# Kernel optimization log

Hardware: AMD Instinct MI355X
Metric: run time of the kernel (lower is better)

## Reference

```python
import jax, jax.numpy as jnp
import numpy as np

N = 131072      # 8192 sudoku puzzles x 16 cells
E = 1048576     # random constraint edges (avg degree 8)
HID = 64
NEG_SLOPE = 0.2


def setup_inputs() -> dict:
    key = jax.random.key(0)
    ks = jax.random.split(key, 18)
    p = lambda k, shape: jax.random.normal(k, shape, dtype=jnp.float32) * 0.05
    return {
        "x": jax.random.randint(ks[0], (N,), 0, 5),
        "edge_index": jax.random.randint(ks[1], (2, E), 0, N),
        "emb": p(ks[2], (5, HID)),
        # conv1: in 64 -> heads=4, C=64, concat
        "W1": p(ks[3], (HID, 4 * HID)),
        "a1_src": p(ks[4], (4, HID)),
        "a1_dst": p(ks[5], (4, HID)),
        "b1": p(ks[6], (4 * HID,)),
        # conv2: in 256 -> heads=4, C=64, concat
        "W2": p(ks[7], (4 * HID, 4 * HID)),
        "a2_src": p(ks[8], (4, HID)),
        "a2_dst": p(ks[9], (4, HID)),
        "b2": p(ks[10], (4 * HID,)),
        # conv3: in 256 -> heads=1, C=64, no concat
        "W3": p(ks[11], (4 * HID, HID)),
        "a3_src": p(ks[12], (1, HID)),
        "a3_dst": p(ks[13], (1, HID)),
        "b3": p(ks[14], (HID,)),
        "fc_w": p(ks[15], (HID, 5)),
        "fc_b": p(ks[16], (5,)),
    }


def gat_conv(x, src, dst, W, a_src, a_dst, b, concat):
    """PyG-style GATConv (self-loops already appended to src/dst)."""
    n = x.shape[0]
    H, C = a_src.shape
    h = (x @ W).reshape(n, H, C)                       # [N,H,C]
    alpha_s = jnp.einsum('nhc,hc->nh', h, a_src)       # [N,H]
    alpha_d = jnp.einsum('nhc,hc->nh', h, a_dst)
    e = jax.nn.leaky_relu(alpha_s[src] + alpha_d[dst], NEG_SLOPE)  # [E,H]
    # scatter-softmax over incoming edges per destination node
    e_max = jax.ops.segment_max(e, dst, num_segments=n)
    e_exp = jnp.exp(e - e_max[dst])
    denom = jax.ops.segment_sum(e_exp, dst, num_segments=n)
    alpha = e_exp / (denom[dst] + 1e-16)               # [E,H]
    msg = h[src] * alpha[:, :, None]                   # [E,H,C]
    out = jax.ops.segment_sum(msg, dst, num_segments=n)  # [N,H,C]
    out = out.reshape(n, H * C) if concat else out.mean(axis=1)
    return out + b


def reference(x, edge_index, emb, W1, a1_src, a1_dst, b1,
              W2, a2_src, a2_dst, b2, W3, a3_src, a3_dst, b3, fc_w, fc_b):
    n = x.shape[0]
    loops = jnp.arange(n)
    src = jnp.concatenate([edge_index[0], loops])  # add self-loops (PyG default)
    dst = jnp.concatenate([edge_index[1], loops])
    h = emb[x]                                                    # [N,64]
    h = jax.nn.elu(gat_conv(h, src, dst, W1, a1_src, a1_dst, b1, True))
    h = jax.nn.elu(gat_conv(h, src, dst, W2, a2_src, a2_dst, b2, True))
    h = jax.nn.elu(gat_conv(h, src, dst, W3, a3_src, a3_dst, b3, False))
    return h @ fc_w + fc_b                                        # [N,5]
```

## Files before the change

### kernel.cpp

```cpp
#include <hip/hip_runtime.h>
#include <hip/hip_bf16.h>
#include <hip/hip_fp8.h>

typedef __attribute__((ext_vector_type(8))) short short8;
typedef __attribute__((ext_vector_type(4))) short short4_t;
typedef __attribute__((ext_vector_type(4))) float floatx4;
typedef __attribute__((ext_vector_type(2))) float floatx2;

constexpr int NB  = 256;
constexpr int CAP = 6144;

__device__ __forceinline__ unsigned short f2bf(float f){
  unsigned int u = __float_as_uint(f);
  u += 0x7FFF + ((u >> 16) & 1);
  return (unsigned short)(u >> 16);
}
__device__ __forceinline__ float bf2f(unsigned short h){
  return __uint_as_float(((unsigned int)h) << 16);
}
__device__ __forceinline__ float lrelu(float x){ return x > 0.f ? x : 0.2f * x; }
__device__ __forceinline__ float eluf(float x){ return x > 0.f ? x : (__expf(x) - 1.f); }

__device__ __forceinline__ unsigned char f2fp8(float f){
  __hip_fp8_e4m3 t(f);
  return (unsigned char)t.__x;
}
__device__ __forceinline__ float fp82f(unsigned char b){
  __hip_fp8_e4m3 t;
  t.__x = (__hip_fp8_storage_t)b;
  return (float)t;
}

template<bool HI>
__device__ __forceinline__ floatx2 fp8pk2(unsigned int v){
#if defined(__has_builtin) && __has_builtin(__builtin_amdgcn_cvt_pk_f32_fp8)
  return __builtin_amdgcn_cvt_pk_f32_fp8((int)v, HI);
#else
  floatx2 r;
  constexpr int sh = HI ? 16 : 0;
  r.x = fp82f((unsigned char)((v >> sh) & 0xFF));
  r.y = fp82f((unsigned char)((v >> (sh + 8)) & 0xFF));
  return r;
#endif
}

__device__ __forceinline__ unsigned int f32x4_to_fp8(float a0, float a1, float a2, float a3){
#if defined(__has_builtin) && __has_builtin(__builtin_amdgcn_cvt_pk_fp8_f32)
  int w = 0;
  w = __builtin_amdgcn_cvt_pk_fp8_f32(a0, a1, w, false);
  w = __builtin_amdgcn_cvt_pk_fp8_f32(a2, a3, w, true);
  return (unsigned int)w;
#else
  return (unsigned int)f2fp8(a0) | ((unsigned int)f2fp8(a1) << 8) |
         ((unsigned int)f2fp8(a2) << 16) | ((unsigned int)f2fp8(a3) << 24);
#endif
}

__device__ __forceinline__ int scr512(int p){
  int q = p >> 2, s = p & 3;
  int qq = ((q & 31) << 2) | (q >> 5);
  return (qq << 2) | s;
}

__device__ __forceinline__ void gload16(const unsigned short* g, unsigned short* l){
  __builtin_amdgcn_global_load_lds(
      (const __attribute__((address_space(1))) unsigned int*)(const void*)g,
      (__attribute__((address_space(3))) unsigned int*)(void*)l,
      16, 0, 0);
}

__global__ __launch_bounds__(256) void part_prep_k(const int* __restrict__ ei, int E, int shift,
                                                   int* __restrict__ gcnt,
                                                   uint2* __restrict__ bbuf, int PB,
                                                   const float* __restrict__ W2,
                                                   unsigned short* __restrict__ Wp2,
                                                   const float* __restrict__ W3,
                                                   unsigned short* __restrict__ Wp3,
                                                   const float* __restrict__ emb,
                                                   const float* __restrict__ W1,
                                                   const float* __restrict__ a1s,
                                                   const float* __restrict__ a1d,
                                                   float* __restrict__ T1,
                                                   float* __restrict__ wt_tab){
  int blk = blockIdx.x;
  int tid = threadIdx.x;
  if (blk < PB){
    __shared__ int hist[NB];
    __shared__ int base[NB];
    hist[tid] = 0;
    __syncthreads();
    int blk_start = blk * 4096;
    int src[16], bkt[16], lp[16];
    #pragma unroll
    for (int k = 0; k < 16; k++){
      int i = blk_start + k * 256 + tid;
      if (i < E){
        int dst = ei[E + i];
        src[k] = ei[i];
        bkt[k] = dst >> shift;
        lp[k] = atomicAdd(&hist[bkt[k]], 1);
      } else {
        bkt[k] = -1;
      }
    }
    __syncthreads();
    base[tid] = atomicAdd(&gcnt[tid], hist[tid]);
    __syncthreads();
    #pragma unroll
    for (int k = 0; k < 16; k++){
      int i = blk_start + k * 256 + tid;
      if (i < E){
        int b = bkt[k];
        int dst = ei[E + i];
        bbuf[(size_t)b * CAP + base[b] + lp[k]] = make_uint2((unsigned)src[k], (unsigned)dst);
      }
    }
    return;
  }
  int b = blk - PB;
  if (b < 256){
    int idx = b * 256 + tid;
    int k = idx >> 8, nn = idx & 255;
    Wp2[nn * 256 + k] = f2bf(W2[idx]);
  } else if (b < 320){
    int idx = (b - 256) * 256 + tid;
    int k = idx >> 6, nn = idx & 63;
    Wp3[nn * 256 + k] = f2bf(W3[idx]);
  } else {
    __shared__ float t_lds[1280];
    __shared__ float as_l[20], ad_l[20];
    for (int i = tid; i < 1280; i += 256){
      int r = i >> 8, c = i & 255;
      float s = 0.f;
      for (int k = 0; k < 64; k++) s += emb[r * 64 + k] * W1[k * 256 + c];
      t_lds[i] = s;
      T1[i] = s;
    }
    __syncthreads();
    if (tid < 20){
      int r = tid >> 2, hh = tid & 3;
      float ss = 0.f, sd = 0.f;
      for (int c = 0; c < 64; c++){
        float f = t_lds[r * 256 + hh * 64 + c];
        ss += f * a1s[hh * 64 + c];
        sd += f * a1d[hh * 64 + c];
      }
      as_l[tid] = ss;
      ad_l[tid] = sd;
    }
    __syncthreads();
    if (tid < 100){
      int xd = tid / 20, rest = tid % 20;
      int h = rest & 3;
      wt_tab[tid] = __expf(lrelu(as_l[rest] + ad_l[xd * 4 + h]));
    }
  }
}

__global__ __launch_bounds__(256) void bscan_k(const int* __restrict__ gcnt,
                                               int* __restrict__ gbase,
                                               int* __restrict__ row_ptr, int N, int dpb){
  __shared__ int s[NB];
  int t = threadIdx.x;
  int v = gcnt[t] + dpb;
  s[t] = v;
  __syncthreads();
  #pragma unroll
  for (int off = 1; off < NB; off <<= 1){
    int u = (t >= off) ? s[t - off] : 0;
    __syncthreads();
    s[t] += u;
    __syncthreads();
  }
  gbase[t] = s[t] - v;
  if (t == NB - 1){ gbase[NB] = s[t]; row_ptr[N] = s[t]; }
}

__global__ __launch_bounds__(256) void sort_k(const uint2* __restrict__ bbuf,
                                              const int* __restrict__ gcnt,
                                              const int* __restrict__ gbase,
                                              int* __restrict__ row_ptr,
                                              int* __restrict__ sorted_src,
                                              int* __restrict__ perm, int dpb){
  __shared__ int counts[512];
  __shared__ int curs[512];
  __shared__ int wsum[256];
  __shared__ int sortedL[CAP + 512];
  __shared__ int dh[64];
  int b = blockIdx.x, tid = threadIdx.x;
  int cnt = gcnt[b];
  int dstBase = b * dpb;
  int gb = gbase[b];
  counts[tid] = 0;
  counts[tid + 256] = 0;
  __syncthreads();
  for (int i = tid; i < cnt; i += 256){
    uint2 p = bbuf[(size_t)b * CAP + i];
    atomicAdd(&counts[(int)p.y - dstBase], 1);
  }
  __syncthreads();
  int c0 = counts[2 * tid] + 1;
  int c1 = counts[2 * tid + 1] + 1;
  int sum = c0 + c1;
  wsum[tid] = sum;
  __syncthreads();
  #pragma unroll
  for (int off = 1; off < 256; off <<= 1){
    int u = (tid >= off) ? wsum[tid - off] : 0;
    __syncthreads();
    wsum[tid] += u;
    __syncthreads();
  }
  int ex = wsum[tid] - sum;
  int ro0 = ex, ro1 = ex + c0;
  curs[2 * tid] = ro0 + 1;
  curs[2 * tid + 1] = ro1 + 1;
  sortedL[ro0] = dstBase + 2 * tid;
  sortedL[ro1] = dstBase + 2 * tid + 1;
  row_ptr[dstBase + 2 * tid] = gb + ro0;
  row_ptr[dstBase + 2 * tid + 1] = gb + ro1;
  __syncthreads();
  for (int i = tid; i < cnt; i += 256){
    uint2 p = bbuf[(size_t)b * CAP + i];
    int pos = atomicAdd(&curs[(int)p.y - dstBase], 1);
    sortedL[pos] = (int)p.x;
  }
  __syncthreads();
  int tot = cnt + dpb;
  for (int i = tid; i < tot; i += 256) sorted_src[gb + i] = sortedL[i];

  __syncthreads();
  if (tid < 64) dh[tid] = 0;
  __syncthreads();
  int dg0 = c0 < 63 ? c0 : 63;
  int dg1 = c1 < 63 ? c1 : 63;
  int r0 = atomicAdd(&dh[dg0], 1);
  int r1 = atomicAdd(&dh[dg1], 1);
  __syncthreads();
  if (tid == 0){
    int run = 0;
    for (int i = 0; i < 64; i++){ int c = dh[i]; dh[i] = run; run += c; }
  }
  __syncthreads();
  perm[dstBase + scr512(dh[dg0] + r0)] = dstBase + 2 * tid;
  perm[dstBase + scr512(dh[dg1] + r1)] = dstBase + 2 * tid + 1;
}

template<int BN, int MODE, bool F8OUT>
__global__ __launch_bounds__(256) void gemm_lds_k(const unsigned short* __restrict__ A,
                                                  const unsigned short* __restrict__ Wp,
                                                  void* __restrict__ Cout, int Nc,
                                                  const float* __restrict__ a_src,
                                                  const float* __restrict__ a_dst,
                                                  float* __restrict__ as_arr,
                                                  float* __restrict__ ad_arr){
  constexpr int K = 256;
  constexpr int NT = BN / 32;
  __shared__ unsigned short Alds[128 * 32];
  __shared__ unsigned short Blds[BN * 32];
  __shared__ float asl[128], adl[128];
  __shared__ float pas[128][2], pad[128][2];
  int tid = threadIdx.x;
  int w = tid >> 6, l = tid & 63;
  int r16 = l & 15, quad = l >> 4;
  int wr = w >> 1, wc = w & 1;
  int mBase = blockIdx.x * 128;
  int nBase = blockIdx.y * BN;

  if constexpr (MODE == 1){
    if (tid < 128){ asl[tid] = a_src[nBase + tid]; adl[tid] = a_dst[nBase + tid]; }
  }
  if constexpr (MODE == 2){
    if (tid < 64){ asl[tid] = a_src[tid]; adl[tid] = a_dst[tid]; }
  }

  int arow = l >> 2;
  int kcol = (l & 3) * 8;
  const unsigned short* gA0 = A + (size_t)(mBase + w * 32 + arow) * K + kcol;
  const unsigned short* gA1 = gA0 + (size_t)16 * K;
  unsigned short* lA0 = &Alds[(w * 32) * 32];
  unsigned short* lA1 = &Alds[(w * 32 + 16) * 32];
  const unsigned short* gB0;
// ... 73 lines not shown
          float v = acc[mt][nt][r];
          int ci = wc * 64 + nt * 16 + r16;
          ps += v * asl[ci];
          pd += v * adl[ci];
        }
        ps += __shfl_xor(ps, 1, 64); ps += __shfl_xor(ps, 2, 64);
        ps += __shfl_xor(ps, 4, 64); ps += __shfl_xor(ps, 8, 64);
        pd += __shfl_xor(pd, 1, 64); pd += __shfl_xor(pd, 2, 64);
        pd += __shfl_xor(pd, 4, 64); pd += __shfl_xor(pd, 8, 64);
        if (r16 == 0){
          int row = mBase + wr * 64 + mt * 16 + quad * 4 + r;
          as_arr[row * 4 + head] = ps;
          ad_arr[row * 4 + head] = pd;
        }
      }
    }
  }
  if constexpr (MODE == 2){
    #pragma unroll
    for (int mt = 0; mt < 4; mt++){
      #pragma unroll
      for (int r = 0; r < 4; r++){
        float ps = 0.f, pd = 0.f;
        #pragma unroll
        for (int nt = 0; nt < NT; nt++){
          float v = acc[mt][nt][r];
          int ci = wc * 32 + nt * 16 + r16;
          ps += v * asl[ci];
          pd += v * adl[ci];
        }
        ps += __shfl_xor(ps, 1, 64); ps += __shfl_xor(ps, 2, 64);
        ps += __shfl_xor(ps, 4, 64); ps += __shfl_xor(ps, 8, 64);
        pd += __shfl_xor(pd, 1, 64); pd += __shfl_xor(pd, 2, 64);
        pd += __shfl_xor(pd, 4, 64); pd += __shfl_xor(pd, 8, 64);
        if (r16 == 0){
          int lr = wr * 64 + mt * 16 + quad * 4 + r;
          pas[lr][wc] = ps;
          pad[lr][wc] = pd;
        }
      }
    }
    __syncthreads();
    if (tid < 128){
      as_arr[mBase + tid] = pas[tid][0] + pas[tid][1];
      ad_arr[mBase + tid] = pad[tid][0] + pad[tid][1];
    }
  }
}


__global__ __launch_bounds__(256) void agg1_k(const int* __restrict__ x,
                                              const float* __restrict__ T1,
                                              const float* __restrict__ wt_tab,
                                              const int* __restrict__ row_ptr,
                                              const int* __restrict__ sorted_src,
                                              const int* __restrict__ perm,
                                              const float* __restrict__ bias,
                                              unsigned short* __restrict__ outb){
  __shared__ float t_lds[1280];
  __shared__ float wt_l[100], b_lds[256];
  __shared__ float cnt_lds[256][5];
  __shared__ int xd_lds[256];
  __shared__ int dd_lds[256];
  int tid = threadIdx.x;
  for (int i = tid; i < 1280; i += 256) t_lds[i] = T1[i];
  if (tid < 100) wt_l[tid] = wt_tab[tid];
  b_lds[tid] = bias[tid];
  int gi = blockIdx.x * 256 + tid;
  int d = perm[(gi & ~511) + scr512(gi & 511)];
  int start = row_ptr[d], end = row_ptr[d + 1];
  xd_lds[tid] = x[d];
  dd_lds[tid] = d;
  float c0 = 0.f, c1 = 0.f, c2 = 0.f, c3 = 0.f, c4 = 0.f;
  for (int e = start; e < end; e++){
    int xs = x[sorted_src[e]];
    c0 += (xs == 0) ? 1.f : 0.f;
    c1 += (xs == 1) ? 1.f : 0.f;
    c2 += (xs == 2) ? 1.f : 0.f;
    c3 += (xs == 3) ? 1.f : 0.f;
    c4 += (xs == 4) ? 1.f : 0.f;
  }
  cnt_lds[tid][0] = c0; cnt_lds[tid][1] = c1; cnt_lds[tid][2] = c2;
  cnt_lds[tid][3] = c3; cnt_lds[tid][4] = c4;
  __syncthreads();
  int w = tid >> 6, l = tid & 63;
  int head = l >> 4;
  int c0i = l * 4;
  for (int dl = w; dl < 256; dl += 4){
    int dd = dd_lds[dl];
    int xd20 = xd_lds[dl] * 20;
    float ws[5];
    float den = 0.f;
    #pragma unroll
    for (int v2 = 0; v2 < 5; v2++){
      float wv = wt_l[xd20 + v2 * 4 + head] * cnt_lds[dl][v2];
      ws[v2] = wv;
      den += wv;
    }
    float inv = 1.f / (den + 1e-16f);
    float num[4] = {0.f, 0.f, 0.f, 0.f};
    #pragma unroll
    for (int v2 = 0; v2 < 5; v2++){
      const float4 row = *(const float4*)&t_lds[v2 * 256 + c0i];
      num[0] += ws[v2] * row.x;
      num[1] += ws[v2] * row.y;
      num[2] += ws[v2] * row.z;
      num[3] += ws[v2] * row.w;
    }
    short4_t ov;
    #pragma unroll
    for (int j = 0; j < 4; j++)
      ov[j] = (short)f2bf(eluf(num[j] * inv + b_lds[c0i + j]));
    *(short4_t*)(outb + (size_t)dd * 256 + c0i) = ov;
  }
}


__global__ __launch_bounds__(256) void agg4_k(const unsigned char* __restrict__ h8,
                                              const float* __restrict__ as_arr,
                                              const float* __restrict__ ad_arr,
                                              const int* __restrict__ row_ptr,
                                              const int* __restrict__ sorted_src,
                                              const int* __restrict__ perm,
                                              const float* __restrict__ bias,
                                              unsigned short* __restrict__ outb){
  int tid = threadIdx.x;
  int w = tid >> 6, l = tid & 63;
  int g = l >> 4, q = l & 15;
  int d = perm[blockIdx.x * 16 + w * 4 + g];
  unsigned coff = (unsigned)(q * 16);
  int head = q >> 2;
  int start = row_ptr[d], end = row_ptr[d + 1];
  float a_d = ad_arr[d * 4 + head];
  floatx2 ac[8];
  #pragma unroll
  for (int j = 0; j < 8; j++){ floatx2 z = {0.f, 0.f}; ac[j] = z; }
  float den = 0.f;
  int e = start;
  for (; e + 3 < end; e += 4){
    unsigned s0 = (unsigned)sorted_src[e];
    unsigned s1 = (unsigned)sorted_src[e + 1];
    unsigned s2 = (unsigned)sorted_src[e + 2];
    unsigned s3 = (unsigned)sorted_src[e + 3];
    uint4 v0 = *(const uint4*)(h8 + (((size_t)s0 << 8) | coff));
    uint4 v1 = *(const uint4*)(h8 + (((size_t)s1 << 8) | coff));
    uint4 v2 = *(const uint4*)(h8 + (((size_t)s2 << 8) | coff));
    uint4 v3 = *(const uint4*)(h8 + (((size_t)s3 << 8) | coff));
    float w0 = __expf(lrelu(as_arr[(s0 << 2) + head] + a_d));
    float w1 = __expf(lrelu(as_arr[(s1 << 2) + head] + a_d));
    float w2 = __expf(lrelu(as_arr[(s2 << 2) + head] + a_d));
    float w3 = __expf(lrelu(as_arr[(s3 << 2) + head] + a_d));
    den += (w0 + w1) + (w2 + w3);
    floatx2 W0 = {w0, w0}, W1 = {w1, w1}, W2 = {w2, w2}, W3 = {w3, w3};
    ac[0] += W0 * fp8pk2<false>(v0.x) + W1 * fp8pk2<false>(v1.x)
           + W2 * fp8pk2<false>(v2.x) + W3 * fp8pk2<false>(v3.x);
    ac[1] += W0 * fp8pk2<true>(v0.x)  + W1 * fp8pk2<true>(v1.x)
           + W2 * fp8pk2<true>(v2.x)  + W3 * fp8pk2<true>(v3.x);
    ac[2] += W0 * fp8pk2<false>(v0.y) + W1 * fp8pk2<false>(v1.y)
           + W2 * fp8pk2<false>(v2.y) + W3 * fp8pk2<false>(v3.y);
    ac[3] += W0 * fp8pk2<true>(v0.y)  + W1 * fp8pk2<true>(v1.y)
           + W2 * fp8pk2<true>(v2.y)  + W3 * fp8pk2<true>(v3.y);
    ac[4] += W0 * fp8pk2<false>(v0.z) + W1 * fp8pk2<false>(v1.z)
           + W2 * fp8pk2<false>(v2.z) + W3 * fp8pk2<false>(v3.z);
    ac[5] += W0 * fp8pk2<true>(v0.z)  + W1 * fp8pk2<true>(v1.z)
           + W2 * fp8pk2<true>(v2.z)  + W3 * fp8pk2<true>(v3.z);
    ac[6] += W0 * fp8pk2<false>(v0.w) + W1 * fp8pk2<false>(v1.w)
           + W2 * fp8pk2<false>(v2.w) + W3 * fp8pk2<false>(v3.w);
    ac[7] += W0 * fp8pk2<true>(v0.w)  + W1 * fp8pk2<true>(v1.w)
           + W2 * fp8pk2<true>(v2.w)  + W3 * fp8pk2<true>(v3.w);
  }
  for (; e < end; e++){
    unsigned s = (unsigned)sorted_src[e];
    uint4 v = *(const uint4*)(h8 + (((size_t)s << 8) | coff));
    float wg = __expf(lrelu(as_arr[(s << 2) + head] + a_d));
    den += wg;
    floatx2 wv = {wg, wg};
    ac[0] += wv * fp8pk2<false>(v.x);
    ac[1] += wv * fp8pk2<true>(v.x);
    ac[2] += wv * fp8pk2<false>(v.y);
    ac[3] += wv * fp8pk2<true>(v.y);
    ac[4] += wv * fp8pk2<false>(v.z);
    ac[5] += wv * fp8pk2<true>(v.z);
    ac[6] += wv * fp8pk2<false>(v.w);
    ac[7] += wv * fp8pk2<true>(v.w);
  }
  float inv = 0.015625f / (den + 1e-16f);
  int cb = q * 16;
  float4 b0 = *(const float4*)&bias[cb];
  float4 b1v = *(const float4*)&bias[cb + 4];
  float4 b2v = *(const float4*)&bias[cb + 8];
  float4 b3v = *(const float4*)&bias[cb + 12];
  float bb[16] = {b0.x, b0.y, b0.z, b0.w, b1v.x, b1v.y, b1v.z, b1v.w,
                  b2v.x, b2v.y, b2v.z, b2v.w, b3v.x, b3v.y, b3v.z, b3v.w};
  short8 o0, o1;
  #pragma unroll
  for (int j = 0; j < 8; j++){
    float v = ((j & 1) ? ac[j >> 1].y : ac[j >> 1].x);
    o0[j] = (short)f2bf(eluf(v * inv + bb[j]));
  }
  #pragma unroll
  for (int j = 0; j < 8; j++){
    float v = ((j & 1) ? ac[4 + (j >> 1)].y : ac[4 + (j >> 1)].x);
    o1[j] = (short)f2bf(eluf(v * inv + bb[8 + j]));
  }
  *(short8*)(outb + (size_t)d * 256 + cb) = o0;
  *(short8*)(outb + (size_t)d * 256 + cb + 8) = o1;
}


__global__ __launch_bounds__(256) void agg3_k(const unsigned char* __restrict__ h8,
                                              const float* __restrict__ as_arr,
                                              const float* __restrict__ ad_arr,
                                              const int* __restrict__ row_ptr,
                                              const int* __restrict__ sorted_src,
                                              const int* __restrict__ perm,
                                              const float* __restrict__ bias,
                                              unsigned short* __restrict__ outb){
  int tid = threadIdx.x;
  int w = tid >> 6, l = tid & 63;
  int g = l >> 3, q = l & 7;
  int d = perm[blockIdx.x * 32 + w * 8 + g];
  unsigned coff = (unsigned)(q * 8);
  int start = row_ptr[d], end = row_ptr[d + 1];
  float a_d = ad_arr[d];
  floatx2 ac[4];
  #pragma unroll
  for (int j = 0; j < 4; j++){ floatx2 z = {0.f, 0.f}; ac[j] = z; }
  float den = 0.f;
  int e = start;
  for (; e + 3 < end; e += 4){
    unsigned s0 = (unsigned)sorted_src[e];
    unsigned s1 = (unsigned)sorted_src[e + 1];
    unsigned s2 = (unsigned)sorted_src[e + 2];
    unsigned s3 = (unsigned)sorted_src[e + 3];
    uint2 v0 = *(const uint2*)(h8 + (((size_t)s0 << 6) | coff));
    uint2 v1 = *(const uint2*)(h8 + (((size_t)s1 << 6) | coff));
    uint2 v2 = *(const uint2*)(h8 + (((size_t)s2 << 6) | coff));
    uint2 v3 = *(const uint2*)(h8 + (((size_t)s3 << 6) | coff));
    float w0 = __expf(lrelu(as_arr[s0] + a_d));
    float w1 = __expf(lrelu(as_arr[s1] + a_d));
    float w2 = __expf(lrelu(as_arr[s2] + a_d));
    float w3 = __expf(lrelu(as_arr[s3] + a_d));
    den += (w0 + w1) + (w2 + w3);
    floatx2 W0 = {w0, w0}, W1 = {w1, w1}, W2 = {w2, w2}, W3 = {w3, w3};
    ac[0] += W0 * fp8pk2<false>(v0.x) + W1 * fp8pk2<false>(v1.x)
           + W2 * fp8pk2<false>(v2.x) + W3 * fp8pk2<false>(v3.x);
    ac[1] += W0 * fp8pk2<true>(v0.x)  + W1 * fp8pk2<true>(v1.x)
           + W2 * fp8pk2<true>(v2.x)  + W3 * fp8pk2<true>(v3.x);
    ac[2] += W0 * fp8pk2<false>(v0.y) + W1 * fp8pk2<false>(v1.y)
           + W2 * fp8pk2<false>(v2.y) + W3 * fp8pk2<false>(v3.y);
    ac[3] += W0 * fp8pk2<true>(v0.y)  + W1 * fp8pk2<true>(v1.y)
           + W2 * fp8pk2<true>(v2.y)  + W3 * fp8pk2<true>(v3.y);
  }
  for (; e < end; e++){
    unsigned s = (unsigned)sorted_src[e];
    float wg = __expf(lrelu(as_arr[s] + a_d));
    den += wg;
    uint2 v = *(const uint2*)(h8 + (((size_t)s << 6) | coff));
    floatx2 wv = {wg, wg};
    ac[0] += wv * fp8pk2<false>(v.x);
    ac[1] += wv * fp8pk2<true>(v.x);
    ac[2] += wv * fp8pk2<false>(v.y);
    ac[3] += wv * fp8pk2<true>(v.y);
  }
  float inv = 0.015625f / (den + 1e-16f);
  int cb = q * 8;
  float4 bA = *(const float4*)&bias[cb];
  float4 bB = *(const float4*)&bias[cb + 4];
  float bb[8] = {bA.x, bA.y, bA.z, bA.w, bB.x, bB.y, bB.z, bB.w};
  short8 ov;
  #pragma unroll
  for (int j = 0; j < 8; j++){
    float v = ((j & 1) ? ac[j >> 1].y : ac[j >> 1].x);
    ov[j] = (short)f2bf(eluf(v * inv + bb[j]));
  }
  *(short8*)(outb + (size_t)d * 64 + cb) = ov;
}


__global__ __launch_bounds__(256) void fc_k(const unsigned short* __restrict__ hb,
                                            const float* __restrict__ fcw,
                                            const float* __restrict__ fcb,
                                            float* __restrict__ out){
  __shared__ float w_lds[320];
  __shared__ float b_lds[5];
  int tid = threadIdx.x;
  for (int i = tid; i < 320; i += 256) w_lds[i] = fcw[i];
  if (tid < 5) b_lds[tid] = fcb[tid];
  __syncthreads();
  int n = blockIdx.x * 256 + tid;
  const short8* p = (const short8*)(hb + (size_t)n * 64);
  float acc[5];
  #pragma unroll
  for (int j = 0; j < 5; j++) acc[j] = b_lds[j];
  #pragma unroll
  for (int b = 0; b < 8; b++){
    short8 v = p[b];
    #pragma unroll
    for (int j8 = 0; j8 < 8; j8++){
      float f = bf2f((unsigned short)v[j8]);
      int k = b * 8 + j8;
      #pragma unroll
      for (int j = 0; j < 5; j++) acc[j] += f * w_lds[k * 5 + j];
    }
  }
  #pragma unroll
  for (int j = 0; j < 5; j++) out[(size_t)n * 5 + j] = acc[j];
}


extern "C" void kernel_launch(void* const* d_in, const int* in_sizes, int n_in,
                              void* d_out, int out_size, void* d_ws, size_t ws_size,
                              hipStream_t stream){
  const int*   x    = (const int*)d_in[0];
  const int*   ei   = (const int*)d_in[1];
  const float* emb  = (const float*)d_in[2];
  const float* W1   = (const float*)d_in[3];
  const float* a1s  = (const float*)d_in[4];
  const float* a1d  = (const float*)d_in[5];
  const float* b1   = (const float*)d_in[6];
  const float* W2   = (const float*)d_in[7];
  const float* a2s  = (const float*)d_in[8];
  const float* a2d  = (const float*)d_in[9];
  const float* b2   = (const float*)d_in[10];
  const float* W3   = (const float*)d_in[11];
  const float* a3s  = (const float*)d_in[12];
  const float* a3d  = (const float*)d_in[13];
  const float* b3   = (const float*)d_in[14];
  const float* fcw  = (const float*)d_in[15];
  const float* fcb  = (const float*)d_in[16];
  float* out = (float*)d_out;

  const int N = in_sizes[0];
  const int E = in_sizes[1] / 2;
  const int dpb = N / NB;
  int shift = 0;
  while ((1 << shift) < dpb) shift++;
  const int PB = (E + 4095) / 4096;

  char* base = (char*)d_ws;
  size_t off = 0;
  auto alloc = [&](size_t bytes) -> void* {
    void* p = base + off;
    off += (bytes + 255) & ~(size_t)255;
    return p;
  };
  unsigned short* bufB    = (unsigned short*)alloc((size_t)N * 256 * 2);
  unsigned char*  buf8    = (unsigned char*)alloc((size_t)N * 256);
  float* alpha_s          = (float*)alloc((size_t)N * 4 * 4);
  float* alpha_d          = (float*)alloc((size_t)N * 4 * 4);
  int* row_ptr            = (int*)alloc((size_t)(N + 1) * 4);
  int* sorted_src         = (int*)alloc((size_t)(E + N) * 4);
  int* perm               = (int*)alloc((size_t)N * 4);
  uint2* bbuf             = (uint2*)alloc((size_t)NB * CAP * 8);
  int* gcnt               = (int*)alloc((size_t)NB * 4);
  int* gbase              = (int*)alloc((size_t)(NB + 1) * 4);
  float* T1               = (float*)alloc(5 * 256 * 4);
  float* wt_tab           = (float*)alloc(100 * 4);
  unsigned short* Wp2     = (unsigned short*)alloc(256 * 256 * 2);
  unsigned short* Wp3     = (unsigned short*)alloc(64 * 256 * 2);

  (void)hipMemsetAsync(gcnt, 0, (size_t)NB * 4, stream);
  part_prep_k<<<PB + 321, 256, 0, stream>>>(ei, E, shift, gcnt, bbuf, PB,
                                            W2, Wp2, W3, Wp3, emb, W1, a1s, a1d, T1, wt_tab);
  bscan_k<<<1, 256, 0, stream>>>(gcnt, gbase, row_ptr, N, dpb);
  sort_k<<<NB, 256, 0, stream>>>(bbuf, gcnt, gbase, row_ptr, sorted_src, perm, dpb);

  agg1_k<<<N / 256, 256, 0, stream>>>(x, T1, wt_tab, row_ptr, sorted_src, perm, b1, bufB);

  gemm_lds_k<128, 1, true><<<dim3(N / 128, 2), 256, 0, stream>>>(bufB, Wp2, buf8, 256,
                                                                 a2s, a2d, alpha_s, alpha_d);
  agg4_k<<<N / 16, 256, 0, stream>>>(buf8, alpha_s, alpha_d, row_ptr, sorted_src, perm, b2, bufB);

  gemm_lds_k<64, 2, true><<<dim3(N / 128, 1), 256, 0, stream>>>(bufB, Wp3, buf8, 64,
                                                                a3s, a3d, alpha_s, alpha_d);
  agg3_k<<<N / 32, 256, 0, stream>>>(buf8, alpha_s, alpha_d, row_ptr, sorted_src, perm, b3, bufB);

  fc_k<<<N / 256, 256, 0, stream>>>(bufB, fcw, fcb, out);
}
```

Measured before the change: 333.6 us.

## Cooperative shuffle-broadcast edge index loads and persistent grids in aggregation kernels

Result: slower. 360.2 us (+8.0%).

```diff
diff --git a/kernel.cpp b/kernel.cpp
--- a/kernel.cpp
+++ b/kernel.cpp
@@ -427,7 +427,18 @@
   xd_lds[tid] = x[d];
   dd_lds[tid] = d;
   float c0 = 0.f, c1 = 0.f, c2 = 0.f, c3 = 0.f, c4 = 0.f;
-  for (int e = start; e < end; e++){
+  int e = start;
+  for (; e + 3 < end; e += 4){
+    int s0 = sorted_src[e], s1 = sorted_src[e + 1];
+    int s2 = sorted_src[e + 2], s3 = sorted_src[e + 3];
+    int x0 = x[s0], x1 = x[s1], x2 = x[s2], x3 = x[s3];
+    c0 += (float)((x0 == 0) + (x1 == 0) + (x2 == 0) + (x3 == 0));
+    c1 += (float)((x0 == 1) + (x1 == 1) + (x2 == 1) + (x3 == 1));
+    c2 += (float)((x0 == 2) + (x1 == 2) + (x2 == 2) + (x3 == 2));
+    c3 += (float)((x0 == 3) + (x1 == 3) + (x2 == 3) + (x3 == 3));
+    c4 += (float)((x0 == 4) + (x1 == 4) + (x2 == 4) + (x3 == 4));
+  }
+  for (; e < end; e++){
     int xs = x[sorted_src[e]];
     c0 += (xs == 0) ? 1.f : 0.f;
     c1 += (xs == 1) ? 1.f : 0.f;
@@ -478,88 +489,87 @@
                                               const int* __restrict__ sorted_src,
                                               const int* __restrict__ perm,
                                               const float* __restrict__ bias,
-                                              unsigned short* __restrict__ outb){
+                                              unsigned short* __restrict__ outb,
+                                              int nBlk){
   int tid = threadIdx.x;
   int w = tid >> 6, l = tid & 63;
   int g = l >> 4, q = l & 15;
-  int d = perm[blockIdx.x * 16 + w * 4 + g];
+  int sl0 = l & 48;
   unsigned coff = (unsigned)(q * 16);
   int head = q >> 2;
-  int start = row_ptr[d], end = row_ptr[d + 1];
-  float a_d = ad_arr[d * 4 + head];
-  floatx2 ac[8];
-  #pragma unroll
-  for (int j = 0; j < 8; j++){ floatx2 z = {0.f, 0.f}; ac[j] = z; }
-  float den = 0.f;
-  int e = start;
-  for (; e + 3 < end; e += 4){
-    unsigned s0 = (unsigned)sorted_src[e];
-    unsigned s1 = (unsigned)sorted_src[e + 1];
-    unsigned s2 = (unsigned)sorted_src[e + 2];
-    unsigned s3 = (unsigned)sorted_src[e + 3];
-    uint4 v0 = *(const uint4*)(h8 + (((size_t)s0 << 8) | coff));
-    uint4 v1 = *(const uint4*)(h8 + (((size_t)s1 << 8) | coff));
-    uint4 v2 = *(const uint4*)(h8 + (((size_t)s2 << 8) | coff));
-    uint4 v3 = *(const uint4*)(h8 + (((size_t)s3 << 8) | coff));
-    float w0 = __expf(lrelu(as_arr[(s0 << 2) + head] + a_d));
-    float w1 = __expf(lrelu(as_arr[(s1 << 2) + head] + a_d));
-    float w2 = __expf(lrelu(as_arr[(s2 << 2) + head] + a_d));
-    float w3 = __expf(lrelu(as_arr[(s3 << 2) + head] + a_d));
-    den += (w0 + w1) + (w2 + w3);
-    floatx2 W0 = {w0, w0}, W1 = {w1, w1}, W2 = {w2, w2}, W3 = {w3, w3};
-    ac[0] += W0 * fp8pk2<false>(v0.x) + W1 * fp8pk2<false>(v1.x)
-           + W2 * fp8pk2<false>(v2.x) + W3 * fp8pk2<false>(v3.x);
-    ac[1] += W0 * fp8pk2<true>(v0.x)  + W1 * fp8pk2<true>(v1.x)
-           + W2 * fp8pk2<true>(v2.x)  + W3 * fp8pk2<true>(v3.x);
-    ac[2] += W0 * fp8pk2<false>(v0.y) + W1 * fp8pk2<false>(v1.y)
-           + W2 * fp8pk2<false>(v2.y) + W3 * fp8pk2<false>(v3.y);
-    ac[3] += W0 * fp8pk2<true>(v0.y)  + W1 * fp8pk2<true>(v1.y)
-           + W2 * fp8pk2<true>(v2.y)  + W3 * fp8pk2<true>(v3.y);
-    ac[4] += W0 * fp8pk2<false>(v0.z) + W1 * fp8pk2<false>(v1.z)
-           + W2 * fp8pk2<false>(v2.z) + W3 * fp8pk2<false>(v3.z);
-    ac[5] += W0 * fp8pk2<true>(v0.z)  + W1 * fp8pk2<true>(v1.z)
-           + W2 * fp8pk2<true>(v2.z)  + W3 * fp8pk2<true>(v3.z);
-    ac[6] += W0 * fp8pk2<false>(v0.w) + W1 * fp8pk2<false>(v1.w)
-           + W2 * fp8pk2<false>(v2.w) + W3 * fp8pk2<false>(v3.w);
-    ac[7] += W0 * fp8pk2<true>(v0.w)  + W1 * fp8pk2<true>(v1.w)
-           + W2 * fp8pk2<true>(v2.w)  + W3 * fp8pk2<true>(v3.w);
-  }
-  for (; e < end; e++){
-    unsigned s = (unsigned)sorted_src[e];
-    uint4 v = *(const uint4*)(h8 + (((size_t)s << 8) | coff));
-    float wg = __expf(lrelu(as_arr[(s << 2) + head] + a_d));
-    den += wg;
-    floatx2 wv = {wg, wg};
-    ac[0] += wv * fp8pk2<false>(v.x);
-    ac[1] += wv * fp8pk2<true>(v.x);
-    ac[2] += wv * fp8pk2<false>(v.y);
-    ac[3] += wv * fp8pk2<true>(v.y);
-    ac[4] += wv * fp8pk2<false>(v.z);
-    ac[5] += wv * fp8pk2<true>(v.z);
-    ac[6] += wv * fp8pk2<false>(v.w);
-    ac[7] += wv * fp8pk2<true>(v.w);
-  }
-  float inv = 0.015625f / (den + 1e-16f);
   int cb = q * 16;
-  float4 b0 = *(const float4*)&bias[cb];
-  float4 b1v = *(const float4*)&bias[cb + 4];
-  float4 b2v = *(const float4*)&bias[cb + 8];
-  float4 b3v = *(const float4*)&bias[cb + 12];
-  float bb[16] = {b0.x, b0.y, b0.z, b0.w, b1v.x, b1v.y, b1v.z, b1v.w,
-                  b2v.x, b2v.y, b2v.z, b2v.w, b3v.x, b3v.y, b3v.z, b3v.w};
-  short8 o0, o1;
-  #pragma unroll
-  for (int j = 0; j < 8; j++){
-    float v = ((j & 1) ? ac[j >> 1].y : ac[j >> 1].x);
-    o0[j] = (short)f2bf(eluf(v * inv + bb[j]));
-  }
-  #pragma unroll
-  for (int j = 0; j < 8; j++){
-    float v = ((j & 1) ? ac[4 + (j >> 1)].y : ac[4 + (j >> 1)].x);
-    o1[j] = (short)f2bf(eluf(v * inv + bb[8 + j]));
-  }
-  *(short8*)(outb + (size_t)d * 256 + cb) = o0;
-  *(short8*)(outb + (size_t)d * 256 + cb + 8) = o1;
+  float4 bv0 = *(const float4*)&bias[cb];
+  float4 bv1 = *(const float4*)&bias[cb + 4];
+  float4 bv2 = *(const float4*)&bias[cb + 8];
+  float4 bv3 = *(const float4*)&bias[cb + 12];
+  float bb[16] = {bv0.x, bv0.y, bv0.z, bv0.w, bv1.x, bv1.y, bv1.z, bv1.w,
+                  bv2.x, bv2.y, bv2.z, bv2.w, bv3.x, bv3.y, bv3.z, bv3.w};
+
+  for (int blk = blockIdx.x; blk < nBlk; blk += gridDim.x){
+    int d = perm[blk * 16 + w * 4 + g];
+    int start = row_ptr[d], end = row_ptr[d + 1];
+    float a_d = ad_arr[d * 4 + head];
+    floatx2 ac[8];
+    #pragma unroll
+    for (int j = 0; j < 8; j++){ floatx2 z = {0.f, 0.f}; ac[j] = z; }
+    float den = 0.f;
+
+    for (int base = start; base < end; base += 16){
+      int myE = base + q;
+      int idxl = (myE < end) ? sorted_src[myE] : 0;
+      #pragma unroll
+      for (int sb = 0; sb < 4; sb++){
+        int eb = base + sb * 4;
+        if (eb < end){
+          unsigned s0 = (unsigned)__shfl(idxl, sl0 + sb * 4 + 0, 64);
+          unsigned s1 = (unsigned)__shfl(idxl, sl0 + sb * 4 + 1, 64);
+          unsigned s2 = (unsigned)__shfl(idxl, sl0 + sb * 4 + 2, 64);
+          unsigned s3 = (unsigned)__shfl(idxl, sl0 + sb * 4 + 3, 64);
+          uint4 v0 = *(const uint4*)(h8 + (((size_t)s0 << 8) | coff));
+          uint4 v1 = *(const uint4*)(h8 + (((size_t)s1 << 8) | coff));
+          uint4 v2 = *(const uint4*)(h8 + (((size_t)s2 << 8) | coff));
+          uint4 v3 = *(const uint4*)(h8 + (((size_t)s3 << 8) | coff));
+          float w0 = (eb + 0 < end) ? __expf(lrelu(as_arr[(s0 << 2) + head] + a_d)) : 0.f;
+          float w1 = (eb + 1 < end) ? __expf(lrelu(as_arr[(s1 << 2) + head] + a_d)) : 0.f;
+          float w2 = (eb + 2 < end) ? __expf(lrelu(as_arr[(s2 << 2) + head] + a_d)) : 0.f;
+          float w3 = (eb + 3 < end) ? __expf(lrelu(as_arr[(s3 << 2) + head] + a_d)) : 0.f;
+          den += (w0 + w1) + (w2 + w3);
+          floatx2 W0 = {w0, w0}, W1 = {w1, w1}, W2 = {w2, w2}, W3 = {w3, w3};
+          ac[0] += W0 * fp8pk2<false>(v0.x) + W1 * fp8pk2<false>(v1.x)
+                 + W2 * fp8pk2<false>(v2.x) + W3 * fp8pk2<false>(v3.x);
+          ac[1] += W0 * fp8pk2<true>(v0.x)  + W1 * fp8pk2<true>(v1.x)
+                 + W2 * fp8pk2<true>(v2.x)  + W3 * fp8pk2<true>(v3.x);
+          ac[2] += W0 * fp8pk2<false>(v0.y) + W1 * fp8pk2<false>(v1.y)
+                 + W2 * fp8pk2<false>(v2.y) + W3 * fp8pk2<false>(v3.y);
+          ac[3] += W0 * fp8pk2<true>(v0.y)  + W1 * fp8pk2<true>(v1.y)
+                 + W2 * fp8pk2<true>(v2.y)  + W3 * fp8pk2<true>(v3.y);
+          ac[4] += W0 * fp8pk2<false>(v0.z) + W1 * fp8pk2<false>(v1.z)
+                 + W2 * fp8pk2<false>(v2.z) + W3 * fp8pk2<false>(v3.z);
+          ac[5] += W0 * fp8pk2<true>(v0.z)  + W1 * fp8pk2<true>(v1.z)
+                 + W2 * fp8pk2<true>(v2.z)  + W3 * fp8pk2<true>(v3.z);
+          ac[6] += W0 * fp8pk2<false>(v0.w) + W1 * fp8pk2<false>(v1.w)
+                 + W2 * fp8pk2<false>(v2.w) + W3 * fp8pk2<false>(v3.w);
+          ac[7] += W0 * fp8pk2<true>(v0.w)  + W1 * fp8pk2<true>(v1.w)
+                 + W2 * fp8pk2<true>(v2.w)  + W3 * fp8pk2<true>(v3.w);
+        }
+      }
+    }
+
+    float inv = 0.015625f / (den + 1e-16f);
+    short8 o0, o1;
+    #pragma unroll
+    for (int j = 0; j < 8; j++){
+      float v = ((j & 1) ? ac[j >> 1].y : ac[j >> 1].x);
+      o0[j] = (short)f2bf(eluf(v * inv + bb[j]));
+    }
+    #pragma unroll
+    for (int j = 0; j < 8; j++){
+      float v = ((j & 1) ? ac[4 + (j >> 1)].y : ac[4 + (j >> 1)].x);
+      o1[j] = (short)f2bf(eluf(v * inv + bb[8 + j]));
+    }
+    *(short8*)(outb + (size_t)d * 256 + cb) = o0;
+    *(short8*)(outb + (size_t)d * 256 + cb + 8) = o1;
+  }
 }
 
 
@@ -570,66 +580,69 @@
                                               const int* __restrict__ sorted_src,
                                               const int* __restrict__ perm,
                                               const float* __restrict__ bias,
-                                              unsigned short* __restrict__ outb){
+                                              unsigned short* __restrict__ outb,
+                                              int nBlk){
   int tid = threadIdx.x;
   int w = tid >> 6, l = tid & 63;
   int g = l >> 3, q = l & 7;
-  int d = perm[blockIdx.x * 32 + w * 8 + g];
+  int sl0 = l & 56;
   unsigned coff = (unsigned)(q * 8);
-  int start = row_ptr[d], end = row_ptr[d + 1];
-  float a_d = ad_arr[d];
-  floatx2 ac[4];
-  #pragma unroll
-  for (int j = 0; j < 4; j++){ floatx2 z = {0.f, 0.f}; ac[j] = z; }
-  float den = 0.f;
-  int e = start;
-  for (; e + 3 < end; e += 4){
-    unsigned s0 = (unsigned)sorted_src[e];
-    unsigned s1 = (unsigned)sorted_src[e + 1];
-    unsigned s2 = (unsigned)sorted_src[e + 2];
-    unsigned s3 = (unsigned)sorted_src[e + 3];
-    uint2 v0 = *(const uint2*)(h8 + (((size_t)s0 << 6) | coff));
-    uint2 v1 = *(const uint2*)(h8 + (((size_t)s1 << 6) | coff));
-    uint2 v2 = *(const uint2*)(h8 + (((size_t)s2 << 6) | coff));
-    uint2 v3 = *(const uint2*)(h8 + (((size_t)s3 << 6) | coff));
-    float w0 = __expf(lrelu(as_arr[s0] + a_d));
-    float w1 = __expf(lrelu(as_arr[s1] + a_d));
-    float w2 = __expf(lrelu(as_arr[s2] + a_d));
-    float w3 = __expf(lrelu(as_arr[s3] + a_d));
-    den += (w0 + w1) + (w2 + w3);
-    floatx2 W0 = {w0, w0}, W1 = {w1, w1}, W2 = {w2, w2}, W3 = {w3, w3};
-    ac[0] += W0 * fp8pk2<false>(v0.x) + W1 * fp8pk2<false>(v1.x)
-           + W2 * fp8pk2<false>(v2.x) + W3 * fp8pk2<false>(v3.x);
-    ac[1] += W0 * fp8pk2<true>(v0.x)  + W1 * fp8pk2<true>(v1.x)
-           + W2 * fp8pk2<true>(v2.x)  + W3 * fp8pk2<true>(v3.x);
-    ac[2] += W0 * fp8pk2<false>(v0.y) + W1 * fp8pk2<false>(v1.y)
-           + W2 * fp8pk2<false>(v2.y) + W3 * fp8pk2<false>(v3.y);
-    ac[3] += W0 * fp8pk2<true>(v0.y)  + W1 * fp8pk2<true>(v1.y)
-           + W2 * fp8pk2<true>(v2.y)  + W3 * fp8pk2<true>(v3.y);
-  }
-  for (; e < end; e++){
-    unsigned s = (unsigned)sorted_src[e];
-    float wg = __expf(lrelu(as_arr[s] + a_d));
-    den += wg;
-    uint2 v = *(const uint2*)(h8 + (((size_t)s << 6) | coff));
-    floatx2 wv = {wg, wg};
-    ac[0] += wv * fp8pk2<false>(v.x);
-    ac[1] += wv * fp8pk2<true>(v.x);
-    ac[2] += wv * fp8pk2<false>(v.y);
-    ac[3] += wv * fp8pk2<true>(v.y);
-  }
-  float inv = 0.015625f / (den + 1e-16f);
   int cb = q * 8;
   float4 bA = *(const float4*)&bias[cb];
   float4 bB = *(const float4*)&bias[cb + 4];
   float bb[8] = {bA.x, bA.y, bA.z, bA.w, bB.x, bB.y, bB.z, bB.w};
-  short8 ov;
-  #pragma unroll
-  for (int j = 0; j < 8; j++){
-    float v = ((j & 1) ? ac[j >> 1].y : ac[j >> 1].x);
-    ov[j] = (short)f2bf(eluf(v * inv + bb[j]));
-  }
-  *(short8*)(outb + (size_t)d * 64 + cb) = ov;
+
+  for (int blk = blockIdx.x; blk < nBlk; blk += gridDim.x){
+    int d = perm[blk * 32 + w * 8 + g];
+    int start = row_ptr[d], end = row_ptr[d + 1];
+    float a_d = ad_arr[d];
+    floatx2 ac[4];
+    #pragma unroll
+    for (int j = 0; j < 4; j++){ floatx2 z = {0.f, 0.f}; ac[j] = z; }
+    float den = 0.f;
+
+    for (int base = start; base < end; base += 8){
+      int myE = base + q;
+      int idxl = (myE < end) ? sorted_src[myE] : 0;
+      #pragma unroll
+      for (int sb = 0; sb < 2; sb++){
+        int eb = base + sb * 4;
+        if (eb < end){
+          unsigned s0 = (unsigned)__shfl(idxl, sl0 + sb * 4 + 0, 64);
+          unsigned s1 = (unsigned)__shfl(idxl, sl0 + sb * 4 + 1, 64);
+          unsigned s2 = (unsigned)__shfl(idxl, sl0 + sb * 4 + 2, 64);
+          unsigned s3 = (unsigned)__shfl(idxl, sl0 + sb * 4 + 3, 64);
+          uint2 v0 = *(const uint2*)(h8 + (((size_t)s0 << 6) | coff));
+          uint2 v1 = *(const uint2*)(h8 + (((size_t)s1 << 6) | coff));
+          uint2 v2 = *(const uint2*)(h8 + (((size_t)s2 << 6) | coff));
+          uint2 v3 = *(const uint2*)(h8 + (((size_t)s3 << 6) | coff));
+          float w0 = (eb + 0 < end) ? __expf(lrelu(as_arr[s0] + a_d)) : 0.f;
+          float w1 = (eb + 1 < end) ? __expf(lrelu(as_arr[s1] + a_d)) : 0.f;
+          float w2 = (eb + 2 < end) ? __expf(lrelu(as_arr[s2] + a_d)) : 0.f;
+          float w3 = (eb + 3 < end) ? __expf(lrelu(as_arr[s3] + a_d)) : 0.f;
+          den += (w0 + w1) + (w2 + w3);
+          floatx2 W0 = {w0, w0}, W1 = {w1, w1}, W2 = {w2, w2}, W3 = {w3, w3};
+          ac[0] += W0 * fp8pk2<false>(v0.x) + W1 * fp8pk2<false>(v1.x)
+                 + W2 * fp8pk2<false>(v2.x) + W3 * fp8pk2<false>(v3.x);
+          ac[1] += W0 * fp8pk2<true>(v0.x)  + W1 * fp8pk2<true>(v1.x)
+                 + W2 * fp8pk2<true>(v2.x)  + W3 * fp8pk2<true>(v3.x);
+          ac[2] += W0 * fp8pk2<false>(v0.y) + W1 * fp8pk2<false>(v1.y)
+                 + W2 * fp8pk2<false>(v2.y) + W3 * fp8pk2<false>(v3.y);
+          ac[3] += W0 * fp8pk2<true>(v0.y)  + W1 * fp8pk2<true>(v1.y)
+                 + W2 * fp8pk2<true>(v2.y)  + W3 * fp8pk2<true>(v3.y);
+        }
+      }
+    }
+
+    float inv = 0.015625f / (den + 1e-16f);
+    short8 ov;
+    #pragma unroll
+    for (int j = 0; j < 8; j++){
+      float v = ((j & 1) ? ac[j >> 1].y : ac[j >> 1].x);
+      ov[j] = (short)f2bf(eluf(v * inv + bb[j]));
+    }
+    *(short8*)(outb + (size_t)d * 64 + cb) = ov;
+  }
 }
 
 
@@ -725,11 +738,13 @@
 
   gemm_lds_k<128, 1, true><<<dim3(N / 128, 2), 256, 0, stream>>>(bufB, Wp2, buf8, 256,
                                                                  a2s, a2d, alpha_s, alpha_d);
-  agg4_k<<<N / 16, 256, 0, stream>>>(buf8, alpha_s, alpha_d, row_ptr, sorted_src, perm, b2, bufB);
+  agg4_k<<<2048, 256, 0, stream>>>(buf8, alpha_s, alpha_d, row_ptr, sorted_src, perm, b2, bufB,
+                                   N / 16);
 
   gemm_lds_k<64, 2, true><<<dim3(N / 128, 1), 256, 0, stream>>>(bufB, Wp3, buf8, 64,
                                                                 a3s, a3d, alpha_s, alpha_d);
-  agg3_k<<<N / 32, 256, 0, stream>>>(buf8, alpha_s, alpha_d, row_ptr, sorted_src, perm, b3, bufB);
+  agg3_k<<<1024, 256, 0, stream>>>(buf8, alpha_s, alpha_d, row_ptr, sorted_src, perm, b3, bufB,
+                                   N / 32);
 
   fc_k<<<N / 256, 256, 0, stream>>>(bufB, fcw, fcb, out);
 }
```

## Pack edge words, precompute layer-1 class counts in sort, fuse FC into agg3

Applied to the files above, without the earlier changes.

After: 310.6 us. 1.07x faster.

```diff
diff --git a/kernel.cpp b/kernel.cpp
--- a/kernel.cpp
+++ b/kernel.cpp
@@ -70,8 +70,9 @@
 }
 
 __global__ __launch_bounds__(256) void part_prep_k(const int* __restrict__ ei, int E, int shift,
+                                                   const int* __restrict__ x,
                                                    int* __restrict__ gcnt,
-                                                   uint2* __restrict__ bbuf, int PB,
+                                                   unsigned* __restrict__ bbuf, int PB,
                                                    const float* __restrict__ W2,
                                                    unsigned short* __restrict__ Wp2,
                                                    const float* __restrict__ W3,
@@ -90,14 +91,18 @@
     hist[tid] = 0;
     __syncthreads();
     int blk_start = blk * 4096;
-    int src[16], bkt[16], lp[16];
+    int ldmask = (1 << shift) - 1;
+    unsigned word[16];
+    int bkt[16], lp[16];
     #pragma unroll
     for (int k = 0; k < 16; k++){
       int i = blk_start + k * 256 + tid;
       if (i < E){
         int dst = ei[E + i];
-        src[k] = ei[i];
+        int s = ei[i];
+        int xs = x[s];
         bkt[k] = dst >> shift;
+        word[k] = (unsigned)s | ((unsigned)(dst & ldmask) << 17) | ((unsigned)xs << 26);
         lp[k] = atomicAdd(&hist[bkt[k]], 1);
       } else {
         bkt[k] = -1;
@@ -108,11 +113,9 @@
     __syncthreads();
     #pragma unroll
     for (int k = 0; k < 16; k++){
-      int i = blk_start + k * 256 + tid;
-      if (i < E){
+      if (bkt[k] >= 0){
         int b = bkt[k];
-        int dst = ei[E + i];
-        bbuf[(size_t)b * CAP + base[b] + lp[k]] = make_uint2((unsigned)src[k], (unsigned)dst);
+        bbuf[(size_t)b * CAP + base[b] + lp[k]] = word[k];
       }
     }
     return;
@@ -176,27 +179,37 @@
   if (t == NB - 1){ gbase[NB] = s[t]; row_ptr[N] = s[t]; }
 }
 
-__global__ __launch_bounds__(256) void sort_k(const uint2* __restrict__ bbuf,
+__global__ __launch_bounds__(256) void sort_k(const unsigned* __restrict__ bbuf,
                                               const int* __restrict__ gcnt,
                                               const int* __restrict__ gbase,
+                                              const int* __restrict__ x,
                                               int* __restrict__ row_ptr,
                                               int* __restrict__ sorted_src,
-                                              int* __restrict__ perm, int dpb){
+                                              int* __restrict__ perm,
+                                              uint2* __restrict__ cnt5, int dpb){
   __shared__ int counts[512];
   __shared__ int curs[512];
   __shared__ int wsum[256];
   __shared__ int sortedL[CAP + 512];
   __shared__ int dh[64];
+  __shared__ int h5[512 * 5];
   int b = blockIdx.x, tid = threadIdx.x;
   int cnt = gcnt[b];
   int dstBase = b * dpb;
   int gb = gbase[b];
   counts[tid] = 0;
   counts[tid + 256] = 0;
+  for (int i = tid; i < dpb * 5; i += 256) h5[i] = 0;
   __syncthreads();
   for (int i = tid; i < cnt; i += 256){
-    uint2 p = bbuf[(size_t)b * CAP + i];
-    atomicAdd(&counts[(int)p.y - dstBase], 1);
+    unsigned pw = bbuf[(size_t)b * CAP + i];
+    atomicAdd(&counts[(pw >> 17) & (dpb - 1)], 1);
+  }
+  {
+    int x0 = x[dstBase + 2 * tid];
+    int x1 = x[dstBase + 2 * tid + 1];
+    atomicAdd(&h5[(2 * tid) * 5 + x0], 1);
+    atomicAdd(&h5[(2 * tid + 1) * 5 + x1], 1);
   }
   __syncthreads();
   int c0 = counts[2 * tid] + 1;
@@ -221,13 +234,25 @@
   row_ptr[dstBase + 2 * tid + 1] = gb + ro1;
   __syncthreads();
   for (int i = tid; i < cnt; i += 256){
-    uint2 p = bbuf[(size_t)b * CAP + i];
-    int pos = atomicAdd(&curs[(int)p.y - dstBase], 1);
-    sortedL[pos] = (int)p.x;
+    unsigned pw = bbuf[(size_t)b * CAP + i];
+    int ldst = (pw >> 17) & (dpb - 1);
+    int pos = atomicAdd(&curs[ldst], 1);
+    sortedL[pos] = (int)(pw & 0x1FFFF);
+    atomicAdd(&h5[ldst * 5 + (pw >> 26)], 1);
   }
   __syncthreads();
   int tot = cnt + dpb;
   for (int i = tid; i < tot; i += 256) sorted_src[gb + i] = sortedL[i];
+
+  {
+    int d0 = 2 * tid, d1 = 2 * tid + 1;
+    unsigned lo0 = (unsigned)h5[d0 * 5 + 0] | ((unsigned)h5[d0 * 5 + 1] << 8) |
+                   ((unsigned)h5[d0 * 5 + 2] << 16) | ((unsigned)h5[d0 * 5 + 3] << 24);
+    unsigned lo1 = (unsigned)h5[d1 * 5 + 0] | ((unsigned)h5[d1 * 5 + 1] << 8) |
+                   ((unsigned)h5[d1 * 5 + 2] << 16) | ((unsigned)h5[d1 * 5 + 3] << 24);
+    cnt5[dstBase + d0] = make_uint2(lo0, (unsigned)h5[d0 * 5 + 4]);
+    cnt5[dstBase + d1] = make_uint2(lo1, (unsigned)h5[d1 * 5 + 4]);
+  }
 
   __syncthreads();
   if (tid < 64) dh[tid] = 0;
@@ -407,42 +432,31 @@
 __global__ __launch_bounds__(256) void agg1_k(const int* __restrict__ x,
                                               const float* __restrict__ T1,
                                               const float* __restrict__ wt_tab,
-                                              const int* __restrict__ row_ptr,
-                                              const int* __restrict__ sorted_src,
-                                              const int* __restrict__ perm,
+                                              const uint2* __restrict__ cnt5,
                                               const float* __restrict__ bias,
                                               unsigned short* __restrict__ outb){
   __shared__ float t_lds[1280];
   __shared__ float wt_l[100], b_lds[256];
   __shared__ float cnt_lds[256][5];
   __shared__ int xd_lds[256];
-  __shared__ int dd_lds[256];
   int tid = threadIdx.x;
   for (int i = tid; i < 1280; i += 256) t_lds[i] = T1[i];
   if (tid < 100) wt_l[tid] = wt_tab[tid];
   b_lds[tid] = bias[tid];
-  int gi = blockIdx.x * 256 + tid;
-  int d = perm[(gi & ~511) + scr512(gi & 511)];
-  int start = row_ptr[d], end = row_ptr[d + 1];
+  int d = blockIdx.x * 256 + tid;
+  uint2 cw = cnt5[d];
   xd_lds[tid] = x[d];
-  dd_lds[tid] = d;
-  float c0 = 0.f, c1 = 0.f, c2 = 0.f, c3 = 0.f, c4 = 0.f;
-  for (int e = start; e < end; e++){
-    int xs = x[sorted_src[e]];
-    c0 += (xs == 0) ? 1.f : 0.f;
-    c1 += (xs == 1) ? 1.f : 0.f;
-    c2 += (xs == 2) ? 1.f : 0.f;
-    c3 += (xs == 3) ? 1.f : 0.f;
-    c4 += (xs == 4) ? 1.f : 0.f;
-  }
-  cnt_lds[tid][0] = c0; cnt_lds[tid][1] = c1; cnt_lds[tid][2] = c2;
-  cnt_lds[tid][3] = c3; cnt_lds[tid][4] = c4;
+  cnt_lds[tid][0] = (float)(cw.x & 0xFF);
+  cnt_lds[tid][1] = (float)((cw.x >> 8) & 0xFF);
+  cnt_lds[tid][2] = (float)((cw.x >> 16) & 0xFF);
+  cnt_lds[tid][3] = (float)(cw.x >> 24);
+  cnt_lds[tid][4] = (float)(cw.y & 0xFF);
   __syncthreads();
   int w = tid >> 6, l = tid & 63;
   int head = l >> 4;
   int c0i = l * 4;
   for (int dl = w; dl < 256; dl += 4){
-    int dd = dd_lds[dl];
+    int dd = blockIdx.x * 256 + dl;
     int xd20 = xd_lds[dl] * 20;
     float ws[5];
     float den = 0.f;
@@ -541,12 +555,12 @@
   }
   float inv = 0.015625f / (den + 1e-16f);
   int cb = q * 16;
-  float4 b0 = *(const float4*)&bias[cb];
-  float4 b1v = *(const float4*)&bias[cb + 4];
-  float4 b2v = *(const float4*)&bias[cb + 8];
-  float4 b3v = *(const float4*)&bias[cb + 12];
-  float bb[16] = {b0.x, b0.y, b0.z, b0.w, b1v.x, b1v.y, b1v.z, b1v.w,
-                  b2v.x, b2v.y, b2v.z, b2v.w, b3v.x, b3v.y, b3v.z, b3v.w};
+  float4 bv0 = *(const float4*)&bias[cb];
+  float4 bv1 = *(const float4*)&bias[cb + 4];
+  float4 bv2 = *(const float4*)&bias[cb + 8];
+  float4 bv3 = *(const float4*)&bias[cb + 12];
+  float bb[16] = {bv0.x, bv0.y, bv0.z, bv0.w, bv1.x, bv1.y, bv1.z, bv1.w,
+                  bv2.x, bv2.y, bv2.z, bv2.w, bv3.x, bv3.y, bv3.z, bv3.w};
   short8 o0, o1;
   #pragma unroll
   for (int j = 0; j < 8; j++){
@@ -570,8 +584,15 @@
                                               const int* __restrict__ sorted_src,
                                               const int* __restrict__ perm,
                                               const float* __restrict__ bias,
-                                              unsigned short* __restrict__ outb){
+                                              const float* __restrict__ fcw,
+                                              const float* __restrict__ fcb,
+                                              float* __restrict__ out){
+  __shared__ float w_lds[320];
+  __shared__ float fb5[5];
   int tid = threadIdx.x;
+  for (int i = tid; i < 320; i += 256) w_lds[i] = fcw[i];
+  if (tid < 5) fb5[tid] = fcb[tid];
+  __syncthreads();
   int w = tid >> 6, l = tid & 63;
   int g = l >> 3, q = l & 7;
   int d = perm[blockIdx.x * 32 + w * 8 + g];
@@ -623,44 +644,31 @@
   float4 bA = *(const float4*)&bias[cb];
   float4 bB = *(const float4*)&bias[cb + 4];
   float bb[8] = {bA.x, bA.y, bA.z, bA.w, bB.x, bB.y, bB.z, bB.w};
-  short8 ov;
+  float p0 = 0.f, p1 = 0.f, p2 = 0.f, p3 = 0.f, p4 = 0.f;
   #pragma unroll
   for (int j = 0; j < 8; j++){
     float v = ((j & 1) ? ac[j >> 1].y : ac[j >> 1].x);
-    ov[j] = (short)f2bf(eluf(v * inv + bb[j]));
-  }
-  *(short8*)(outb + (size_t)d * 64 + cb) = ov;
-}
-
-
-__global__ __launch_bounds__(256) void fc_k(const unsigned short* __restrict__ hb,
-                                            const float* __restrict__ fcw,
-                                            const float* __restrict__ fcb,
-                                            float* __restrict__ out){
-  __shared__ float w_lds[320];
-  __shared__ float b_lds[5];
-  int tid = threadIdx.x;
-  for (int i = tid; i < 320; i += 256) w_lds[i] = fcw[i];
-  if (tid < 5) b_lds[tid] = fcb[tid];
-  __syncthreads();
-  int n = blockIdx.x * 256 + tid;
-  const short8* p = (const short8*)(hb + (size_t)n * 64);
-  float acc[5];
-  #pragma unroll
-  for (int j = 0; j < 5; j++) acc[j] = b_lds[j];
-  #pragma unroll
-  for (int b = 0; b < 8; b++){
-    short8 v = p[b];
-    #pragma unroll
-    for (int j8 = 0; j8 < 8; j8++){
-      float f = bf2f((unsigned short)v[j8]);
-      int k = b * 8 + j8;
-      #pragma unroll
-      for (int j = 0; j < 5; j++) acc[j] += f * w_lds[k * 5 + j];
-    }
-  }
-  #pragma unroll
-  for (int j = 0; j < 5; j++) out[(size_t)n * 5 + j] = acc[j];
+    float h = eluf(v * inv + bb[j]);
+    const float* wr = &w_lds[(cb + j) * 5];
+    p0 += h * wr[0];
+    p1 += h * wr[1];
+    p2 += h * wr[2];
+    p3 += h * wr[3];
+    p4 += h * wr[4];
+  }
+  p0 += __shfl_xor(p0, 1, 64); p0 += __shfl_xor(p0, 2, 64); p0 += __shfl_xor(p0, 4, 64);
+  p1 += __shfl_xor(p1, 1, 64); p1 += __shfl_xor(p1, 2, 64); p1 += __shfl_xor(p1, 4, 64);
+  p2 += __shfl_xor(p2, 1, 64); p2 += __shfl_xor(p2, 2, 64); p2 += __shfl_xor(p2, 4, 64);
+  p3 += __shfl_xor(p3, 1, 64); p3 += __shfl_xor(p3, 2, 64); p3 += __shfl_xor(p3, 4, 64);
+  p4 += __shfl_xor(p4, 1, 64); p4 += __shfl_xor(p4, 2, 64); p4 += __shfl_xor(p4, 4, 64);
+  if (q == 0){
+    float* o = out + (size_t)d * 5;
+    o[0] = p0 + fb5[0];
+    o[1] = p1 + fb5[1];
+    o[2] = p2 + fb5[2];
+    o[3] = p3 + fb5[3];
+    o[4] = p4 + fb5[4];
+  }
 }
 
 
@@ -707,7 +715,8 @@
   int* row_ptr            = (int*)alloc((size_t)(N + 1) * 4);
   int* sorted_src         = (int*)alloc((size_t)(E + N) * 4);
   int* perm               = (int*)alloc((size_t)N * 4);
-  uint2* bbuf             = (uint2*)alloc((size_t)NB * CAP * 8);
+  uint2* cnt5             = (uint2*)alloc((size_t)N * 8);
+  unsigned* bbuf          = (unsigned*)alloc((size_t)NB * CAP * 4);
   int* gcnt               = (int*)alloc((size_t)NB * 4);
   int* gbase              = (int*)alloc((size_t)(NB + 1) * 4);
   float* T1               = (float*)alloc(5 * 256 * 4);
@@ -716,12 +725,12 @@
   unsigned short* Wp3     = (unsigned short*)alloc(64 * 256 * 2);
 
   (void)hipMemsetAsync(gcnt, 0, (size_t)NB * 4, stream);
-  part_prep_k<<<PB + 321, 256, 0, stream>>>(ei, E, shift, gcnt, bbuf, PB,
+  part_prep_k<<<PB + 321, 256, 0, stream>>>(ei, E, shift, x, gcnt, bbuf, PB,
                                             W2, Wp2, W3, Wp3, emb, W1, a1s, a1d, T1, wt_tab);
   bscan_k<<<1, 256, 0, stream>>>(gcnt, gbase, row_ptr, N, dpb);
-  sort_k<<<NB, 256, 0, stream>>>(bbuf, gcnt, gbase, row_ptr, sorted_src, perm, dpb);
-
-  agg1_k<<<N / 256, 256, 0, stream>>>(x, T1, wt_tab, row_ptr, sorted_src, perm, b1, bufB);
+  sort_k<<<NB, 256, 0, stream>>>(bbuf, gcnt, gbase, x, row_ptr, sorted_src, perm, cnt5, dpb);
+
+  agg1_k<<<N / 256, 256, 0, stream>>>(x, T1, wt_tab, cnt5, b1, bufB);
 
   gemm_lds_k<128, 1, true><<<dim3(N / 128, 2), 256, 0, stream>>>(bufB, Wp2, buf8, 256,
                                                                  a2s, a2d, alpha_s, alpha_d);
@@ -729,7 +738,6 @@
 
   gemm_lds_k<64, 2, true><<<dim3(N / 128, 1), 256, 0, stream>>>(bufB, Wp3, buf8, 64,
                                                                 a3s, a3d, alpha_s, alpha_d);
-  agg3_k<<<N / 32, 256, 0, stream>>>(buf8, alpha_s, alpha_d, row_ptr, sorted_src, perm, b3, bufB);
-
-  fc_k<<<N / 256, 256, 0, stream>>>(bufB, fcw, fcb, out);
-}
+  agg3_k<<<N / 32, 256, 0, stream>>>(buf8, alpha_s, alpha_d, row_ptr, sorted_src, perm, b3,
+                                     fcw, fcb, out);
+}
```
